# Kernel optimization log

Hardware: AMD Instinct MI355X
Metric: run time of the kernel (lower is better)

The kernel has to match this reference:

```python
import jax, jax.numpy as jnp
import numpy as np

N_NODES = 50000
N_EDGES = 800000
D_FEAT = 128
EMBED = 128


def setup_inputs() -> dict:
    key = jax.random.key(0)
    ks = jax.random.split(key, 6)
    node_features = jax.random.normal(ks[0], (N_NODES, D_FEAT), dtype=jnp.float32)
    senders = jax.random.randint(ks[1], (N_EDGES,), 0, N_NODES, dtype=jnp.int32)
    receivers = jax.random.randint(ks[2], (N_EDGES,), 0, N_NODES, dtype=jnp.int32)
    edge_features = jax.random.normal(ks[3], (N_EDGES, D_FEAT), dtype=jnp.float32)
    # xavier-normal-ish scaled params
    W = jax.random.normal(ks[4], (D_FEAT, 2 * EMBED), dtype=jnp.float32) * (2.0 / (D_FEAT + 2 * EMBED)) ** 0.5
    W_e = jax.random.normal(ks[5], (D_FEAT, EMBED), dtype=jnp.float32) * (2.0 / (D_FEAT + EMBED)) ** 0.5
    b_W = jnp.zeros((2 * EMBED,), dtype=jnp.float32)
    b_We = jnp.zeros((EMBED,), dtype=jnp.float32)
    return dict(node_features=node_features, senders=senders, receivers=receivers,
                edge_features=edge_features, W=W, b_W=b_W, W_e=W_e, b_We=b_We)


def reference(node_features, senders, receivers, edge_features, W, b_W, W_e, b_We):
    num_nodes = node_features.shape[-2]
    # dense proj then split into self (xi) and neighbor (xj) halves
    h = node_features @ W + b_W              # [N, 2*E]
    xi, xj = jnp.split(h, 2, axis=-1)        # [N, E] each
    # gather neighbor messages per edge
    xji = xj[senders]                         # [E, E]
    xji = xji + (edge_features @ W_e + b_We)  # edge feature contribution
    # degree normalization
    in_degree = jax.ops.segment_sum(jnp.ones_like(receivers, dtype=xji.dtype), receivers, num_segments=num_nodes)
    xji = xji / (in_degree[receivers][..., None] + 1e-6)
    nodes = xi + jax.ops.segment_sum(xji, receivers, num_segments=num_nodes)
    return nodes
```

## Files before the change

### kernel.cpp

```cpp
#include <hip/hip_runtime.h>

#define NN 50000
#define NE 800000
#define DF 128
#define BM 32
#define NB ((NN + BM - 1) / BM)
#define SCAN_B ((NN + 255) / 256)
#define GB ((NN + 63) / 64)
#define HB ((NE + 255) / 256)

typedef __attribute__((ext_vector_type(8))) short bf16x8;
typedef __attribute__((ext_vector_type(4))) float f32x4;
typedef __attribute__((ext_vector_type(2))) float f32x2;

static const size_t OFF_DEG  = 0;
static const size_t OFF_OFFS = 204800;
static const size_t OFF_PART = 409600;
static const size_t OFF_RANK = 614400;
static const size_t OFF_CSR  = 3814400;
static const size_t OFF_BCTA = 10214400;
static const size_t OFF_W2T  = 10279936;
static const size_t OFF_P2   = 10312704;

__device__ __forceinline__ unsigned f2bf(float f) {
    unsigned u = __float_as_uint(f);
    return (u + 0x7FFFu + ((u >> 16) & 1u)) >> 16;
}
__device__ __forceinline__ f32x2 ntload2(const float* p) {
    return __builtin_nontemporal_load(reinterpret_cast<const f32x2*>(p));
}

__global__ void k_setup(const float* __restrict__ W, const float* __restrict__ We,
                        unsigned* __restrict__ deg, unsigned short* __restrict__ BcTa,
                        unsigned short* __restrict__ W2T) {
    int idx = blockIdx.x * blockDim.x + threadIdx.x;
    if (idx < NN) deg[idx] = 0;
    if (idx < 128 * 256) {
        int col = idx >> 8, k = idx & 255;
        float v = (k < 128) ? W[k * 256 + col] : We[(k - 128) * 128 + col];
        BcTa[idx] = (unsigned short)f2bf(v);
    }
    if (idx < 128 * 128) {
        int col = idx >> 7, k = idx & 127;
        W2T[idx] = (unsigned short)f2bf(W[k * 256 + 128 + col]);
    }
}

__global__ __launch_bounds__(256) void k_gemm1hist(
    const float* __restrict__ X, const unsigned short* __restrict__ W2T,
    unsigned short* __restrict__ P2, const int* __restrict__ rcv,
    unsigned* __restrict__ deg, unsigned* __restrict__ rank) {
    __shared__ unsigned short As[64 * 128];
    if (blockIdx.x >= GB) {
        int e = (blockIdx.x - GB) * 256 + threadIdx.x;
        if (e < NE) rank[e] = atomicAdd(&deg[rcv[e]], 1u);
        return;
    }
    const int tid = threadIdx.x;
    const int w = tid >> 6, lane = tid & 63;
    const int l15 = lane & 15, l4 = lane >> 4;
    const int m0 = blockIdx.x * 64;
    char* Asb = (char*)As;

    for (int i = tid; i < 64 * 32; i += 256) {
        int r = i >> 5, g = i & 31;
        int n = m0 + r;
        f32x4 v = {0.f, 0.f, 0.f, 0.f};
        if (n < NN) v = *reinterpret_cast<const f32x4*>(X + (size_t)n * DF + g * 4);
        unsigned pk0 = f2bf(v[0]) | (f2bf(v[1]) << 16);
        unsigned pk1 = f2bf(v[2]) | (f2bf(v[3]) << 16);
        unsigned byte = (unsigned)(r * 256 + g * 8) ^ ((unsigned)(r & 7) << 4);
        *reinterpret_cast<uint2*>(Asb + byte) = make_uint2(pk0, pk1);
    }
    __syncthreads();

    const int rrow = w * 16 + l15;
    const unsigned rswz = (unsigned)(rrow & 7) << 4;
    f32x4 acc[8];
#pragma unroll
    for (int ng = 0; ng < 8; ++ng) acc[ng] = (f32x4){0.f, 0.f, 0.f, 0.f};
#pragma unroll
    for (int kk = 0; kk < 4; ++kk) {
        unsigned abyte = (unsigned)(rrow * 256 + (kk * 32 + l4 * 8) * 2) ^ rswz;
        bf16x8 a = *reinterpret_cast<const bf16x8*>(Asb + abyte);
#pragma unroll
        for (int ng = 0; ng < 8; ++ng) {
            bf16x8 b = *reinterpret_cast<const bf16x8*>(
                W2T + (size_t)(ng * 16 + l15) * 128 + kk * 32 + l4 * 8);
            acc[ng] = __builtin_amdgcn_mfma_f32_16x16x32_bf16(a, b, acc[ng], 0, 0, 0);
        }
    }
#pragma unroll
    for (int ng = 0; ng < 8; ++ng) {
        int col = ng * 16 + l15;
#pragma unroll
        for (int j = 0; j < 4; ++j) {
            int row = m0 + w * 16 + l4 * 4 + j;
            if (row < NN) P2[(size_t)row * DF + col] = (unsigned short)f2bf(acc[ng][j]);
        }
    }
}

__global__ void k_scan1(const unsigned* __restrict__ deg, unsigned* __restrict__ part) {
    int idx = blockIdx.x * 256 + threadIdx.x;
    unsigned v = (idx < NN) ? deg[idx] : 0;
#pragma unroll
    for (int o = 32; o; o >>= 1) v += __shfl_down(v, o);
    __shared__ unsigned wsum[4];
    int w = threadIdx.x >> 6, lane = threadIdx.x & 63;
    if (lane == 0) wsum[w] = v;
    __syncthreads();
    if (threadIdx.x == 0) part[blockIdx.x] = wsum[0] + wsum[1] + wsum[2] + wsum[3];
}

__global__ void k_scan3(const unsigned* __restrict__ deg, const unsigned* __restrict__ part,
                        unsigned* __restrict__ offs) {
    const int b = blockIdx.x;
    int idx = b * 256 + threadIdx.x;
    unsigned v = (idx < NN) ? deg[idx] : 0;
    int w = threadIdx.x >> 6, lane = threadIdx.x & 63;
    unsigned x = v;
#pragma unroll
    for (int o = 1; o < 64; o <<= 1) {
        unsigned y = __shfl_up(x, o);
        if (lane >= o) x += y;
    }
    __shared__ unsigned wsum[4];
    __shared__ unsigned base_s;
    if (lane == 63) wsum[w] = x;
    if (w == 0) {
        unsigned s = 0;
        for (int i = lane; i < b; i += 64) s += part[i];
#pragma unroll
        for (int o = 32; o; o >>= 1) s += __shfl_down(s, o);
        if (lane == 0) base_s = s;
    }
    __syncthreads();
    unsigned base = base_s;
    for (int i = 0; i < w; ++i) base += wsum[i];
    if (idx < NN) offs[idx] = base + x - v;
    if (b == SCAN_B - 1 && threadIdx.x == 255) offs[NN] = base + x;
}

__global__ void k_scatter(const int* __restrict__ snd, const int* __restrict__ rcv,
                          const unsigned* __restrict__ offs, const unsigned* __restrict__ rank,
                          int2* __restrict__ csr) {
    int e = blockIdx.x * blockDim.x + threadIdx.x;
    if (e >= NE) return;
    csr[offs[rcv[e]] + rank[e]] = make_int2(snd[e], e);
}

__global__ __launch_bounds__(512) void k_aggemm(
    const float* __restrict__ X, const float* __restrict__ EF,
    const unsigned short* __restrict__ P2, const unsigned* __restrict__ offs,
    const int2* __restrict__ csr, const unsigned short* __restrict__ BcTa,
    const float* __restrict__ bW, const float* __restrict__ bWe,
    float* __restrict__ out) {
    __shared__ unsigned short As[BM * 256];
    __shared__ float XJ[BM][132];
    __shared__ float cf_s[BM];
    const int tid = threadIdx.x;
    const int w = tid >> 6, lane = tid & 63;
    const int m0 = blockIdx.x * BM;
    char* Asb = (char*)As;

    for (int i = tid; i < BM * 32; i += 512) {
        int r = i >> 5, g = i & 31;
        int n = m0 + r;
        f32x4 v = {0.f, 0.f, 0.f, 0.f};
        if (n < NN) v = *reinterpret_cast<const f32x4*>(X + (size_t)n * DF + g * 4);
        unsigned pk0 = f2bf(v[0]) | (f2bf(v[1]) << 16);
        unsigned pk1 = f2bf(v[2]) | (f2bf(v[3]) << 16);
        unsigned byte = (unsigned)(r * 512 + g * 8) ^ ((unsigned)(r & 7) << 4);
        *reinterpret_cast<uint2*>(Asb + byte) = make_uint2(pk0, pk1);
    }

    {
        const int l2 = lane * 2;
        for (int t = 0; t < 4; ++t) {
            int r = w * 4 + t;
            int n = m0 + r;
            unsigned s0 = 0, s1 = 0;
            if (n < NN) { s0 = offs[n]; s1 = offs[n + 1]; }
            s0 = __builtin_amdgcn_readfirstlane(s0);
            s1 = __builtin_amdgcn_readfirstlane(s1);
            unsigned dg = s1 - s0;
            float efa = 0.f, efb = 0.f, xja = 0.f, xjb = 0.f;
            unsigned nb = (dg + 7) >> 3;
            unsigned p = s0;
            for (unsigned bdy = 0; bdy < nb; ++bdy, p += 8) {
#pragma unroll
                for (int i = 0; i < 8; ++i) {
                    unsigned pe = p + i;
                    bool act = pe < s1;
                    unsigned pc = act ? pe : s0;
                    int2 se = csr[pc];
                    f32x2 ev = ntload2(EF + (size_t)se.y * DF + l2);
                    unsigned pu = *reinterpret_cast<const unsigned*>(
                        P2 + (size_t)se.x * DF + l2);
                    float m = act ? 1.f : 0.f;
                    efa += m * ev[0]; efb += m * ev[1];
                    xja += m * __uint_as_float(pu << 16);
                    xjb += m * __uint_as_float(pu & 0xFFFF0000u);
                }
            }
            float dgf = (float)dg;
            float inv = 1.0f / (dgf + 1e-6f);
            unsigned pk = f2bf(efa * inv) | (f2bf(efb * inv) << 16);
            unsigned byte = (unsigned)(r * 512 + 256 + lane * 4) ^ ((unsigned)(r & 7) << 4);
            *reinterpret_cast<unsigned*>(Asb + byte) = pk;
            *reinterpret_cast<float2*>(&XJ[r][l2]) = make_float2(xja * inv, xjb * inv);
            if (lane == 0) cf_s[r] = dgf * inv;
        }
    }
    __syncthreads();

    {
        const int l15 = lane & 15, l4 = lane >> 4;
        const int h = w & 1;
        const int rrow = h * 16 + l15;
        const int n0 = (w >> 1) * 32;
        f32x4 acc0 = {0.f, 0.f, 0.f, 0.f}, acc1 = {0.f, 0.f, 0.f, 0.f};
        const unsigned rswz = (unsigned)(rrow & 7) << 4;
#pragma unroll
        for (int kk = 0; kk < 8; ++kk) {
            unsigned abyte = (unsigned)(rrow * 512 + (kk * 32 + l4 * 8) * 2) ^ rswz;
            bf16x8 a = *reinterpret_cast<const bf16x8*>(Asb + abyte);
            bf16x8 b0 = *reinterpret_cast<const bf16x8*>(
                BcTa + (size_t)(n0 + l15) * 256 + kk * 32 + l4 * 8);
            bf16x8 b1 = *reinterpret_cast<const bf16x8*>(
                BcTa + (size_t)(n0 + 16 + l15) * 256 + kk * 32 + l4 * 8);
            acc0 = __builtin_amdgcn_mfma_f32_16x16x32_bf16(a, b0, acc0, 0, 0, 0);
            acc1 = __builtin_amdgcn_mfma_f32_16x16x32_bf16(a, b1, acc1, 0, 0, 0);
        }
#pragma unroll
        for (int ng = 0; ng < 2; ++ng) {
            int col = n0 + ng * 16 + l15;
            float bx = bW[col];
            float bj = bW[128 + col] + bWe[col];
            f32x4 acc = ng ? acc1 : acc0;
#pragma unroll
            for (int j = 0; j < 4; ++j) {
                int lr = h * 16 + l4 * 4 + j;
                int row = m0 + lr;
                if (row < NN) {
                    float o = acc[j] + XJ[lr][col] + bx + cf_s[lr] * bj;
                    __builtin_nontemporal_store(o, &out[(size_t)row * DF + col]);
                }
            }
        }
    }
}

extern "C" void kernel_launch(void* const* d_in, const int* in_sizes, int n_in,
                              void* d_out, int out_size, void* d_ws, size_t ws_size,
                              hipStream_t stream) {
    const float* X   = (const float*)d_in[0];
    const int*   snd = (const int*)d_in[1];
    const int*   rcv = (const int*)d_in[2];
    const float* EF  = (const float*)d_in[3];
    const float* W   = (const float*)d_in[4];
    const float* bW  = (const float*)d_in[5];
    const float* We  = (const float*)d_in[6];
    const float* bWe = (const float*)d_in[7];
    float* out = (float*)d_out;

    char* ws = (char*)d_ws;
    unsigned* deg  = (unsigned*)(ws + OFF_DEG);
    unsigned* offs = (unsigned*)(ws + OFF_OFFS);
    unsigned* part = (unsigned*)(ws + OFF_PART);
    unsigned* rank = (unsigned*)(ws + OFF_RANK);
    int2*     csr  = (int2*)(ws + OFF_CSR);
    unsigned short* BcTa = (unsigned short*)(ws + OFF_BCTA);
    unsigned short* W2T  = (unsigned short*)(ws + OFF_W2T);
    unsigned short* P2   = (unsigned short*)(ws + OFF_P2);

    k_setup<<<(NN + 255) / 256, 256, 0, stream>>>(W, We, deg, BcTa, W2T);
    k_gemm1hist<<<GB + HB, 256, 0, stream>>>(X, W2T, P2, rcv, deg, rank);
    k_scan1<<<SCAN_B, 256, 0, stream>>>(deg, part);
    k_scan3<<<SCAN_B, 256, 0, stream>>>(deg, part, offs);
    k_scatter<<<(NE + 255) / 256, 256, 0, stream>>>(snd, rcv, offs, rank, csr);
    k_aggemm<<<NB, 512, 0, stream>>>(X, EF, P2, offs, csr, BcTa, bW, bWe, out);
}
```

Measured before the change: 196.1 us.

## Fuse scan and CSR scatter into one cooperative kernel; vectorize CSR loads

Replaces the three launches for partial sums, prefix scan and CSR scatter with a single cooperative kernel of 1024 blocks that uses grid-wide syncs between phases and a grid-stride loop for the scatter. The goal is to cut kernel launch gaps and inter-kernel drain overhead. Separately, the aggregation loop now loads eight CSR entries as two 32-byte blocks per batch instead of eight individual int2 loads. The block loads can read past s1 into the next node's or unwritten CSR slots, and those entries are masked. Cooperative launch adds grid-sync cost and requires all 1024 blocks to be co-resident.

New measurement: 422.6 us. 2.15x slower.

```diff
diff --git a/kernel.cpp b/kernel.cpp
--- a/kernel.cpp
+++ b/kernel.cpp
@@ -1,4 +1,7 @@
 #include <hip/hip_runtime.h>
+#include <hip/hip_cooperative_groups.h>
+
+namespace cg = cooperative_groups;
 
 #define NN 50000
 #define NE 800000
@@ -8,6 +11,7 @@
 #define SCAN_B ((NN + 255) / 256)
 #define GB ((NN + 63) / 64)
 #define HB ((NE + 255) / 256)
+#define COOP_B 1024
 
 typedef __attribute__((ext_vector_type(8))) short bf16x8;
 typedef __attribute__((ext_vector_type(4))) float f32x4;
@@ -29,6 +33,8 @@
 __device__ __forceinline__ f32x2 ntload2(const float* p) {
     return __builtin_nontemporal_load(reinterpret_cast<const f32x2*>(p));
 }
+
+struct __attribute__((aligned(8))) CsrBlk { int2 e[4]; };
 
 __global__ void k_setup(const float* __restrict__ W, const float* __restrict__ We,
                         unsigned* __restrict__ deg, unsigned short* __restrict__ BcTa,
@@ -101,53 +107,57 @@
     }
 }
 
-__global__ void k_scan1(const unsigned* __restrict__ deg, unsigned* __restrict__ part) {
-    int idx = blockIdx.x * 256 + threadIdx.x;
-    unsigned v = (idx < NN) ? deg[idx] : 0;
-#pragma unroll
-    for (int o = 32; o; o >>= 1) v += __shfl_down(v, o);
-    __shared__ unsigned wsum[4];
-    int w = threadIdx.x >> 6, lane = threadIdx.x & 63;
-    if (lane == 0) wsum[w] = v;
-    __syncthreads();
-    if (threadIdx.x == 0) part[blockIdx.x] = wsum[0] + wsum[1] + wsum[2] + wsum[3];
-}
-
-__global__ void k_scan3(const unsigned* __restrict__ deg, const unsigned* __restrict__ part,
-                        unsigned* __restrict__ offs) {
+__global__ __launch_bounds__(256) void k_csr(
+    const unsigned* __restrict__ deg, unsigned* __restrict__ part,
+    unsigned* __restrict__ offs, const int* __restrict__ snd,
+    const int* __restrict__ rcv, const unsigned* __restrict__ rank,
+    int2* __restrict__ csr) {
+    cg::grid_group grid = cg::this_grid();
     const int b = blockIdx.x;
-    int idx = b * 256 + threadIdx.x;
-    unsigned v = (idx < NN) ? deg[idx] : 0;
-    int w = threadIdx.x >> 6, lane = threadIdx.x & 63;
-    unsigned x = v;
-#pragma unroll
-    for (int o = 1; o < 64; o <<= 1) {
-        unsigned y = __shfl_up(x, o);
-        if (lane >= o) x += y;
-    }
-    __shared__ unsigned wsum[4];
-    __shared__ unsigned base_s;
-    if (lane == 63) wsum[w] = x;
-    if (w == 0) {
-        unsigned s = 0;
-        for (int i = lane; i < b; i += 64) s += part[i];
-#pragma unroll
-        for (int o = 32; o; o >>= 1) s += __shfl_down(s, o);
-        if (lane == 0) base_s = s;
-    }
-    __syncthreads();
-    unsigned base = base_s;
-    for (int i = 0; i < w; ++i) base += wsum[i];
-    if (idx < NN) offs[idx] = base + x - v;
-    if (b == SCAN_B - 1 && threadIdx.x == 255) offs[NN] = base + x;
-}
-
-__global__ void k_scatter(const int* __restrict__ snd, const int* __restrict__ rcv,
-                          const unsigned* __restrict__ offs, const unsigned* __restrict__ rank,
-                          int2* __restrict__ csr) {
-    int e = blockIdx.x * blockDim.x + threadIdx.x;
-    if (e >= NE) return;
-    csr[offs[rcv[e]] + rank[e]] = make_int2(snd[e], e);
+    const int tid = threadIdx.x;
+    const int w = tid >> 6, lane = tid & 63;
+
+    if (b < SCAN_B) {
+        int idx = b * 256 + tid;
+        unsigned v = (idx < NN) ? deg[idx] : 0;
+#pragma unroll
+        for (int o = 32; o; o >>= 1) v += __shfl_down(v, o);
+        __shared__ unsigned wsum1[4];
+        if (lane == 0) wsum1[w] = v;
+        __syncthreads();
+        if (tid == 0) part[b] = wsum1[0] + wsum1[1] + wsum1[2] + wsum1[3];
+    }
+    grid.sync();
+
+    if (b < SCAN_B) {
+        int idx = b * 256 + tid;
+        unsigned v = (idx < NN) ? deg[idx] : 0;
+        unsigned x = v;
+#pragma unroll
+        for (int o = 1; o < 64; o <<= 1) {
+            unsigned y = __shfl_up(x, o);
+            if (lane >= o) x += y;
+        }
+        __shared__ unsigned wsum[4];
+        __shared__ unsigned base_s;
+        if (lane == 63) wsum[w] = x;
+        if (w == 0) {
+            unsigned s = 0;
+            for (int i = lane; i < b; i += 64) s += part[i];
+#pragma unroll
+            for (int o = 32; o; o >>= 1) s += __shfl_down(s, o);
+            if (lane == 0) base_s = s;
+        }
+        __syncthreads();
+        unsigned base = base_s;
+        for (int i = 0; i < w; ++i) base += wsum[i];
+        if (idx < NN) offs[idx] = base + x - v;
+        if (b == SCAN_B - 1 && tid == 255) offs[NN] = base + x;
+    }
+    grid.sync();
+
+    for (int e = b * 256 + tid; e < NE; e += COOP_B * 256)
+        csr[offs[rcv[e]] + rank[e]] = make_int2(snd[e], e);
 }
 
 __global__ __launch_bounds__(512) void k_aggemm(
@@ -189,12 +199,14 @@
             unsigned nb = (dg + 7) >> 3;
             unsigned p = s0;
             for (unsigned bdy = 0; bdy < nb; ++bdy, p += 8) {
+                CsrBlk bA = *reinterpret_cast<const CsrBlk*>(csr + p);
+                CsrBlk bB = *reinterpret_cast<const CsrBlk*>(csr + p + 4);
+                int2 safe = bA.e[0];
 #pragma unroll
                 for (int i = 0; i < 8; ++i) {
-                    unsigned pe = p + i;
-                    bool act = pe < s1;
-                    unsigned pc = act ? pe : s0;
-                    int2 se = csr[pc];
+                    bool act = p + i < s1;
+                    int2 se = (i < 4) ? bA.e[i] : bB.e[i - 4];
+                    se = act ? se : safe;
                     f32x2 ev = ntload2(EF + (size_t)se.y * DF + l2);
                     unsigned pu = *reinterpret_cast<const unsigned*>(
                         P2 + (size_t)se.x * DF + l2);
@@ -277,8 +289,17 @@
 
     k_setup<<<(NN + 255) / 256, 256, 0, stream>>>(W, We, deg, BcTa, W2T);
     k_gemm1hist<<<GB + HB, 256, 0, stream>>>(X, W2T, P2, rcv, deg, rank);
-    k_scan1<<<SCAN_B, 256, 0, stream>>>(deg, part);
-    k_scan3<<<SCAN_B, 256, 0, stream>>>(deg, part, offs);
-    k_scatter<<<(NE + 255) / 256, 256, 0, stream>>>(snd, rcv, offs, rank, csr);
+
+    {
+        const unsigned* deg_c = deg;
+        const int* snd_c = snd;
+        const int* rcv_c = rcv;
+        const unsigned* rank_c = rank;
+        void* args[] = {(void*)&deg_c, (void*)&part, (void*)&offs,
+                        (void*)&snd_c, (void*)&rcv_c, (void*)&rank_c, (void*)&csr};
+        hipLaunchCooperativeKernel((void*)k_csr, dim3(COOP_B), dim3(256),
+                                   args, 0, stream);
+    }
+
     k_aggemm<<<NB, 512, 0, stream>>>(X, EF, P2, offs, csr, BcTa, bW, bWe, out);
 }
```
